# Kernel tuning notes

Hardware: AMD Instinct MI355X
Metric: run time of the kernel (lower is better)

The kernel has to match this reference:

```python
import jax, jax.numpy as jnp
import numpy as np

B, T, C = 4, 2048, 1024
H = 16
HS = C // H

def setup_inputs() -> dict:
    key = jax.random.key(0)
    ks = jax.random.split(key, 5)
    s = 0.02
    return {
        "x": jax.random.normal(ks[0], (B, T, C), dtype=jnp.float32),
        "c_attn_w": jax.random.normal(ks[1], (C, 3 * C), dtype=jnp.float32) * s,
        "c_attn_b": jax.random.normal(ks[2], (3 * C,), dtype=jnp.float32) * s,
        "c_proj_w": jax.random.normal(ks[3], (C, C), dtype=jnp.float32) * s,
        "c_proj_b": jax.random.normal(ks[4], (C,), dtype=jnp.float32) * s,
    }

def reference(x, c_attn_w, c_attn_b, c_proj_w, c_proj_b):
    b, t, c = x.shape
    qkv = x @ c_attn_w + c_attn_b                       # (B,T,3C)
    q, k, v = jnp.split(qkv, 3, axis=2)
    # (B,T,C) -> (B,H,T,hs)
    q = q.reshape(b, t, H, HS).transpose(0, 2, 1, 3)
    k = k.reshape(b, t, H, HS).transpose(0, 2, 1, 3)
    v = v.reshape(b, t, H, HS).transpose(0, 2, 1, 3)
    scale = 1.0 / np.sqrt(HS).astype(np.float32)
    attn = jnp.einsum("bhqd,bhkd->bhqk", q, k) * scale  # (B,H,T,T)
    causal = jnp.tril(jnp.ones((t, t), dtype=bool))
    attn = jnp.where(causal[None, None, :, :], attn, -jnp.inf)
    attn = jax.nn.softmax(attn, axis=-1)
    y = jnp.einsum("bhqk,bhkd->bhqd", attn, v)          # (B,H,T,hs)
    y = y.transpose(0, 2, 1, 3).reshape(b, t, c)        # (B,T,C)
    return y @ c_proj_w + c_proj_b
```

## Files before the change

kernel.cpp:

```cpp
#include <hip/hip_runtime.h>

typedef __attribute__((ext_vector_type(8))) _Float16 h8;
typedef __attribute__((ext_vector_type(4))) _Float16 h4;
typedef __attribute__((ext_vector_type(4))) float f4;
typedef __attribute__((ext_vector_type(16))) float f16x;
typedef __attribute__((ext_vector_type(4))) unsigned u4;

#define MFMA16(a,b,c) __builtin_amdgcn_mfma_f32_16x16x32_f16(a,b,c,0,0,0)
#define MFMA32(a,b,c) __builtin_amdgcn_mfma_f32_32x32x16_f16(a,b,c,0,0,0)

__device__ inline void gload16(const void* g, void* l) {
    __builtin_amdgcn_global_load_lds(
        (const __attribute__((address_space(1))) void*)g,
        (__attribute__((address_space(3))) void*)l, 16, 0, 0);
}

__device__ inline float swap_half(float x) { return __shfl_xor(x, 32, 64); }

__global__ __launch_bounds__(256) void k_f32_to_f16(const float* __restrict__ in,
                                                    _Float16* __restrict__ out, int n4) {
    int i = blockIdx.x * 256 + threadIdx.x;
    if (i < n4) {
        float4 v = ((const float4*)in)[i];
        h4 h;
        h[0] = (_Float16)v.x; h[1] = (_Float16)v.y;
        h[2] = (_Float16)v.z; h[3] = (_Float16)v.w;
        ((h4*)out)[i] = h;
    }
}

__global__ __launch_bounds__(256) void k_transpose_f16(const float* __restrict__ W,
                                                       _Float16* __restrict__ Wt,
                                                       int K, int N) {
    __shared__ float tile[64 * 68];
    const int k0 = blockIdx.x * 64, n0 = blockIdx.y * 64;
    const int t = threadIdx.x;
    const int tr = t >> 4;
    const int tc = t & 15;
#pragma unroll
    for (int i = 0; i < 4; ++i) {
        int r = tr + i * 16;
        float4 v = *(const float4*)(W + (size_t)(k0 + r) * N + n0 + tc * 4);
        *(float4*)(&tile[r * 68 + tc * 4]) = v;
    }
    __syncthreads();
#pragma unroll
    for (int i = 0; i < 4; ++i) {
        int nl = tr + i * 16;
        h4 hv;
#pragma unroll
        for (int j = 0; j < 4; ++j)
            hv[j] = (_Float16)tile[(tc * 4 + j) * 68 + nl];
        *(h4*)(Wt + (size_t)(n0 + nl) * K + k0 + tc * 4) = hv;
    }
}

template <int MODE>
__global__ __launch_bounds__(256) void k_gemm(const _Float16* __restrict__ A,
                                              const _Float16* __restrict__ Bt,
                                              const float* __restrict__ bias,
                                              _Float16* __restrict__ oQ,
                                              _Float16* __restrict__ oK,
                                              _Float16* __restrict__ oV,
                                              float* __restrict__ oF,
                                              int M, int N, int K) {
    __shared__ _Float16 As[2][128 * 32];
    __shared__ _Float16 Bs[2][128 * 32];
    const int tid = threadIdx.x;
    const int lane = tid & 63, wv = tid >> 6;
    const int wm = wv >> 1, wn = wv & 1;
    const int l15 = lane & 15, l4 = lane >> 4;
    const int bm = blockIdx.x * 128, bn = blockIdx.y * 128;
    f4 acc[4][4] = {};

    const int srow = lane >> 2, scol = (lane & 3) * 8;
    const _Float16* Ag = A + (size_t)(bm + srow) * K + scol;
    const _Float16* Bg = Bt + (size_t)(bn + srow) * K + scol;

#pragma unroll
    for (int j = 0; j < 2; ++j) {
        const int rb_ = (wv * 2 + j) * 16;
        gload16(Ag + (size_t)rb_ * K, &As[0][(wv * 2 + j) * 512]);
        gload16(Bg + (size_t)rb_ * K, &Bs[0][(wv * 2 + j) * 512]);
    }
    asm volatile("s_waitcnt vmcnt(0)" ::: "memory");
    __syncthreads();

    int cur = 0;
    for (int k0 = 0; k0 < K; k0 += 32) {
        if (k0 + 32 < K) {
#pragma unroll
            for (int j = 0; j < 2; ++j) {
                const int rb_ = (wv * 2 + j) * 16;
                gload16(Ag + (size_t)rb_ * K + k0 + 32, &As[cur ^ 1][(wv * 2 + j) * 512]);
                gload16(Bg + (size_t)rb_ * K + k0 + 32, &Bs[cur ^ 1][(wv * 2 + j) * 512]);
            }
        }

        const _Float16* Ac = As[cur];
        const _Float16* Bc = Bs[cur];
        h8 af[4], bf[4];
#pragma unroll
        for (int i = 0; i < 4; ++i)
            af[i] = *(const h8*)(&Ac[(wm * 64 + i * 16 + l15) * 32 + l4 * 8]);
#pragma unroll
        for (int i = 0; i < 4; ++i)
            bf[i] = *(const h8*)(&Bc[(wn * 64 + i * 16 + l15) * 32 + l4 * 8]);
        __builtin_amdgcn_s_setprio(1);
#pragma unroll
        for (int mi = 0; mi < 4; ++mi)
#pragma unroll
            for (int ni = 0; ni < 4; ++ni)
                acc[mi][ni] = MFMA16(af[mi], bf[ni], acc[mi][ni]);
        __builtin_amdgcn_s_setprio(0);

        asm volatile("s_waitcnt vmcnt(0)" ::: "memory");
        __syncthreads();
        cur ^= 1;
    }

#pragma unroll
    for (int mi = 0; mi < 4; ++mi) {
#pragma unroll
        for (int ni = 0; ni < 4; ++ni) {
            int col = bn + wn * 64 + ni * 16 + l15;
            float bv = bias[col];
            int rb = bm + wm * 64 + mi * 16 + l4 * 4;
            if (MODE == 0) {
                int which = col >> 10, n1 = col & 1023;
                int hh = n1 >> 6, dd = n1 & 63;
                if (which == 2) {
                    int b = rb >> 11, tq = rb & 2047;
                    h4 pv;
#pragma unroll
                    for (int i = 0; i < 4; ++i) pv[i] = (_Float16)(acc[mi][ni][i] + bv);
                    *(h4*)(oV + ((size_t)(b * 16 + hh) * 64 + dd) * 2048 + tq) = pv;
                } else {
                    _Float16* dst = which == 0 ? oQ : oK;
                    const float scl = which == 0 ? 0.18033688011112042f : 1.0f;
#pragma unroll
                    for (int i = 0; i < 4; ++i) {
                        int row = rb + i;
                        int b = row >> 11, tq = row & 2047;
                        dst[(((size_t)b * 16 + hh) * 2048 + tq) * 64 + dd] =
                            (_Float16)((acc[mi][ni][i] + bv) * scl);
                    }
                }
            } else {
#pragma unroll
                for (int i = 0; i < 4; ++i)
                    oF[(size_t)(rb + i) * N + col] = acc[mi][ni][i] + bv;
            }
        }
    }
}

#define SWZI(row, cb) ((((row) << 7) + ((cb) ^ ((((row) & 7) << 4)))) >> 1)

__global__ __launch_bounds__(64) void k_attn(const _Float16* __restrict__ Qh,
                                             const _Float16* __restrict__ Kh,
                                             const _Float16* __restrict__ Vt,
                                             _Float16* __restrict__ Yh) {
    __shared__ _Float16 lds[8192];
    const int bid = blockIdx.x;
    const int bh = bid & 63;
    const int qb = 63 - (bid >> 6);
    const int t = threadIdx.x;
    const int l31 = t & 31, hi = t >> 5;
    const int h16 = hi * 16, h4o = hi * 4;
    const size_t base = (size_t)bh * 2048 * 64;

    const int qabs = qb * 32 + l31;
    h8 qf[4];
#pragma unroll
    for (int dk = 0; dk < 4; ++dk)
        qf[dk] = *(const h8*)(Qh + base + (size_t)qabs * 64 + dk * 16 + hi * 8);

    f16x O0 = {}, O1 = {};
    float m = -1e30f, l = 0.f;

    const int sr = t >> 3;
    const int sc = (t & 7) * 8;
    const _Float16* Kg = Kh + base + (size_t)sr * 64 + sc;
    const _Float16* Vg = Vt + base + (size_t)sr * 2048 + sc;
    const int kbw = qb >> 1;

    {
        h8 kn[8], vn[8];
#pragma unroll
        for (int j = 0; j < 8; ++j) kn[j] = *(const h8*)(Kg + j * 512);
#pragma unroll
        for (int j = 0; j < 8; ++j) vn[j] = *(const h8*)(Vg + j * 16384);
#pragma unroll
        for (int j = 0; j < 8; ++j) *(h8*)(&lds[SWZI(j * 8 + sr, (t & 7) * 16)]) = kn[j];
#pragma unroll
        for (int j = 0; j < 8; ++j) *(h8*)(&lds[4096 + SWZI(j * 8 + sr, (t & 7) * 16)]) = vn[j];
    }
    asm volatile("s_waitcnt lgkmcnt(0)" ::: "memory");
    __builtin_amdgcn_sched_barrier(0);

    for (int kb = 0; kb <= kbw; ++kb) {
        const bool pre = (kb < kbw);
        h8 kn[8], vn[8];
        if (pre) {
#pragma unroll
            for (int j = 0; j < 8; ++j)
                kn[j] = *(const h8*)(Kg + (size_t)(kb + 1) * 4096 + j * 512);
        }

        f16x S0 = {}, S1 = {};
        __builtin_amdgcn_s_setprio(1);
#pragma unroll
        for (int dk = 0; dk < 4; ++dk) {
            h8 kf0 = *(const h8*)(&lds[SWZI(l31, dk * 32 + h16)]);
            h8 kf1 = *(const h8*)(&lds[SWZI(32 + l31, dk * 32 + h16)]);
            S0 = MFMA32(kf0, qf[dk], S0);
            S1 = MFMA32(kf1, qf[dk], S1);
        }
        __builtin_amdgcn_s_setprio(0);

        if (pre) {
#pragma unroll
            for (int j = 0; j < 8; ++j)
                vn[j] = *(const h8*)(Vg + (size_t)(kb + 1) * 64 + j * 16384);
        }

        if (kb == kbw) {
#pragma unroll
            for (int r = 0; r < 16; ++r) {
                int key = kb * 64 + (r & 3) + 8 * (r >> 2) + h4o;
                if (key > qabs) S0[r] = -1e30f;
                if (key + 32 > qabs) S1[r] = -1e30f;
            }
        }

        float tr[16];
#pragma unroll
        for (int r = 0; r < 16; ++r) tr[r] = fmaxf(S0[r], S1[r]);
#pragma unroll
        for (int st = 8; st >= 1; st >>= 1)
#pragma unroll
            for (int r = 0; r < st; ++r) tr[r] = fmaxf(tr[r], tr[r + st]);
        float pm = fmaxf(tr[0], swap_half(tr[0]));
        if (!__all(pm - m <= 8.f)) {
            float mnew = fmaxf(m, pm);
            float scl = __builtin_amdgcn_exp2f(m - mnew);
            m = mnew;
            l *= scl;
#pragma unroll
            for (int r = 0; r < 16; ++r) { O0[r] *= scl; O1[r] *= scl; }
        }
#pragma unroll
        for (int r = 0; r < 16; ++r) {
            S0[r] = __builtin_amdgcn_exp2f(S0[r] - m);
            S1[r] = __builtin_amdgcn_exp2f(S1[r] - m);
        }
#pragma unroll
        for (int r = 0; r < 16; ++r) tr[r] = S0[r] + S1[r];
#pragma unroll
        for (int st = 8; st >= 1; st >>= 1)
#pragma unroll
            for (int r = 0; r < st; ++r) tr[r] += tr[r + st];
        l += tr[0] + swap_half(tr[0]);

        h8 pb[4];
#pragma unroll
        for (int kk = 0; kk < 4; ++kk) {
            const int bb = (kk & 1) * 8;
            unsigned W0, W1, W2, W3;
            if (kk < 2) {
                W0 = __builtin_bit_cast(unsigned, __builtin_amdgcn_cvt_pkrtz(S0[bb + 0], S0[bb + 1]));
                W1 = __builtin_bit_cast(unsigned, __builtin_amdgcn_cvt_pkrtz(S0[bb + 2], S0[bb + 3]));
                W2 = __builtin_bit_cast(unsigned, __builtin_amdgcn_cvt_pkrtz(S0[bb + 4], S0[bb + 5]));
                W3 = __builtin_bit_cast(unsigned, __builtin_amdgcn_cvt_pkrtz(S0[bb + 6], S0[bb + 7]));
            } else {
                W0 = __builtin_bit_cast(unsigned, __builtin_amdgcn_cvt_pkrtz(S1[bb + 0], S1[bb + 1]));
                W1 = __builtin_bit_cast(unsigned, __builtin_amdgcn_cvt_pkrtz(S1[bb + 2], S1[bb + 3]));
                W2 = __builtin_bit_cast(unsigned, __builtin_amdgcn_cvt_pkrtz(S1[bb + 4], S1[bb + 5]));
                W3 = __builtin_bit_cast(unsigned, __builtin_amdgcn_cvt_pkrtz(S1[bb + 6], S1[bb + 7]));
            }
            unsigned E0 = (unsigned)__shfl_xor((int)(hi ? W0 : W2), 32, 64);
            unsigned E1 = (unsigned)__shfl_xor((int)(hi ? W1 : W3), 32, 64);
            u4 wvv;
            wvv[0] = hi ? E0 : W0;
            wvv[1] = hi ? E1 : W1;
            wvv[2] = hi ? W2 : E0;
            wvv[3] = hi ? W3 : E1;
            pb[kk] = __builtin_bit_cast(h8, wvv);
        }

        __builtin_amdgcn_s_setprio(1);
#pragma unroll
        for (int kk = 0; kk < 4; ++kk) {
            h8 vf0 = *(const h8*)(&lds[4096 + SWZI(l31, kk * 32 + h16)]);
            h8 vf1 = *(const h8*)(&lds[4096 + SWZI(32 + l31, kk * 32 + h16)]);
            O0 = MFMA32(vf0, pb[kk], O0);
            O1 = MFMA32(vf1, pb[kk], O1);
        }
        __builtin_amdgcn_s_setprio(0);

        if (pre) {
            asm volatile("s_waitcnt lgkmcnt(0)" ::: "memory");
            __builtin_amdgcn_sched_barrier(0);
#pragma unroll
            for (int j = 0; j < 8; ++j) *(h8*)(&lds[SWZI(j * 8 + sr, (t & 7) * 16)]) = kn[j];
#pragma unroll
            for (int j = 0; j < 8; ++j) *(h8*)(&lds[4096 + SWZI(j * 8 + sr, (t & 7) * 16)]) = vn[j];
        }
    }

    asm volatile("s_waitcnt lgkmcnt(0)" ::: "memory");
    __builtin_amdgcn_sched_barrier(0);
    {
        float inv = 1.0f / l;
        _Float16* ow = (_Float16*)lds + (size_t)l31 * 72;
#pragma unroll
        for (int rr = 0; rr < 4; ++rr) {
            h4 a, b;
#pragma unroll
            for (int q = 0; q < 4; ++q) {
                a[q] = (_Float16)(O0[rr * 4 + q] * inv);
                b[q] = (_Float16)(O1[rr * 4 + q] * inv);
            }
            *(h4*)(&ow[rr * 8 + h4o]) = a;
            *(h4*)(&ow[32 + rr * 8 + h4o]) = b;
        }
    }
    asm volatile("s_waitcnt lgkmcnt(0)" ::: "memory");
    __builtin_amdgcn_sched_barrier(0);
    {
        const int b = bh >> 4, head = bh & 15;
        const int row = t >> 1;
#pragma unroll
        for (int i = 0; i < 4; ++i) {
            int seg = (t & 1) * 4 + i;
            h8 v = *(const h8*)(&lds[row * 72 + seg * 8]);
            *(h8*)(Yh + ((size_t)(b * 2048 + qb * 32 + row)) * 1024 + head * 64 + seg * 8) = v;
        }
    }
}

extern "C" void kernel_launch(void* const* d_in, const int* in_sizes, int n_in,
                              void* d_out, int out_size, void* d_ws, size_t ws_size,
                              hipStream_t stream) {
    const float* x  = (const float*)d_in[0];
    const float* Wa = (const float*)d_in[1];
    const float* ba = (const float*)d_in[2];
    const float* Wp = (const float*)d_in[3];
    const float* bp = (const float*)d_in[4];
    float* out = (float*)d_out;

    _Float16* ws = (_Float16*)d_ws;
    const size_t SZ_X = (size_t)8192 * 1024;
    const size_t SZ_WA = (size_t)3072 * 1024;
    const size_t SZ_WP = (size_t)1024 * 1024;
    const size_t SZ_H = (size_t)64 * 2048 * 64;
    _Float16* xh  = ws;
    _Float16* WaT = xh + SZ_X;
    _Float16* WpT = WaT + SZ_WA;
    _Float16* Qh  = WpT + SZ_WP;
    _Float16* Kh  = Qh + SZ_H;
    _Float16* Vth = Kh + SZ_H;
    _Float16* Yh  = Vth + SZ_H;

    k_f32_to_f16<<<8192, 256, 0, stream>>>(x, xh, (int)(SZ_X / 4));
    k_transpose_f16<<<dim3(16, 48), 256, 0, stream>>>(Wa, WaT, 1024, 3072);
    k_transpose_f16<<<dim3(16, 16), 256, 0, stream>>>(Wp, WpT, 1024, 1024);
    k_gemm<0><<<dim3(64, 24), 256, 0, stream>>>(xh, WaT, ba, Qh, Kh, Vth, nullptr,
                                                8192, 3072, 1024);
    k_attn<<<4096, 64, 0, stream>>>(Qh, Kh, Vth, Yh);
    k_gemm<1><<<dim3(64, 8), 256, 0, stream>>>(Yh, WpT, bp, nullptr, nullptr, nullptr,
                                               out, 8192, 1024, 1024);
}
```

Baseline: 188.1 us.

## Share K/V tiles across four waves per attention block with 128-query tiles

The attention kernel moves from one 64-thread wave handling 32 queries to a 256-thread block of four waves covering 128 queries. The waves cooperatively load each 64-key K/V tile into LDS and share it, which cuts redundant global K/V traffic by up to fourfold. In exchange it adds __syncthreads barriers per key tile, and waves whose causal range ends earlier sit idle through the final tiles. The output staging is also switched to a swizzled LDS layout for 128 rows.

```diff
diff --git a/kernel.cpp b/kernel.cpp
--- a/kernel.cpp
+++ b/kernel.cpp
@@ -157,20 +157,20 @@
 
 #define SWZI(row, cb) ((((row) << 7) + ((cb) ^ ((((row) & 7) << 4)))) >> 1)
 
-__global__ __launch_bounds__(64) void k_attn(const _Float16* __restrict__ Qh,
-                                             const _Float16* __restrict__ Kh,
-                                             const _Float16* __restrict__ Vt,
-                                             _Float16* __restrict__ Yh) {
+__global__ __launch_bounds__(256) void k_attn(const _Float16* __restrict__ Qh,
+                                              const _Float16* __restrict__ Kh,
+                                              const _Float16* __restrict__ Vt,
+                                              _Float16* __restrict__ Yh) {
     __shared__ _Float16 lds[8192];
     const int bid = blockIdx.x;
     const int bh = bid & 63;
-    const int qb = 63 - (bid >> 6);
-    const int t = threadIdx.x;
-    const int l31 = t & 31, hi = t >> 5;
+    const int qt = 15 - (bid >> 6);
+    const int tid = threadIdx.x, w = tid >> 6;
+    const int l31 = tid & 31, hi = (tid >> 5) & 1;
     const int h16 = hi * 16, h4o = hi * 4;
     const size_t base = (size_t)bh * 2048 * 64;
 
-    const int qabs = qb * 32 + l31;
+    const int qabs = qt * 128 + w * 32 + l31;
     h8 qf[4];
 #pragma unroll
     for (int dk = 0; dk < 4; ++dk)
@@ -179,141 +179,140 @@
     f16x O0 = {}, O1 = {};
     float m = -1e30f, l = 0.f;
 
-    const int sr = t >> 3;
-    const int sc = (t & 7) * 8;
-    const _Float16* Kg = Kh + base + (size_t)sr * 64 + sc;
-    const _Float16* Vg = Vt + base + (size_t)sr * 2048 + sc;
-    const int kbw = qb >> 1;
+    const int sr = tid >> 3;
+    const int sc8 = (tid & 7) * 8;
+    const int scb = (tid & 7) * 16;
+    const int kbb = 2 * qt + 1;
+    const int kbw = 2 * qt + (w >> 1);
 
     {
-        h8 kn[8], vn[8];
-#pragma unroll
-        for (int j = 0; j < 8; ++j) kn[j] = *(const h8*)(Kg + j * 512);
-#pragma unroll
-        for (int j = 0; j < 8; ++j) vn[j] = *(const h8*)(Vg + j * 16384);
-#pragma unroll
-        for (int j = 0; j < 8; ++j) *(h8*)(&lds[SWZI(j * 8 + sr, (t & 7) * 16)]) = kn[j];
-#pragma unroll
-        for (int j = 0; j < 8; ++j) *(h8*)(&lds[4096 + SWZI(j * 8 + sr, (t & 7) * 16)]) = vn[j];
-    }
-    asm volatile("s_waitcnt lgkmcnt(0)" ::: "memory");
-    __builtin_amdgcn_sched_barrier(0);
-
-    for (int kb = 0; kb <= kbw; ++kb) {
-        const bool pre = (kb < kbw);
-        h8 kn[8], vn[8];
+#pragma unroll
+        for (int j = 0; j < 2; ++j) {
+            int row = j * 32 + sr;
+            h8 kv = *(const h8*)(Kh + base + (size_t)row * 64 + sc8);
+            h8 vv = *(const h8*)(Vt + base + (size_t)row * 2048 + sc8);
+            *(h8*)(&lds[SWZI(row, scb)]) = kv;
+            *(h8*)(&lds[4096 + SWZI(row, scb)]) = vv;
+        }
+    }
+    __syncthreads();
+
+    for (int kb = 0; kb <= kbb; ++kb) {
+        const bool pre = (kb < kbb);
+        h8 kn[2], vn[2];
         if (pre) {
 #pragma unroll
-            for (int j = 0; j < 8; ++j)
-                kn[j] = *(const h8*)(Kg + (size_t)(kb + 1) * 4096 + j * 512);
-        }
-
-        f16x S0 = {}, S1 = {};
-        __builtin_amdgcn_s_setprio(1);
-#pragma unroll
-        for (int dk = 0; dk < 4; ++dk) {
-            h8 kf0 = *(const h8*)(&lds[SWZI(l31, dk * 32 + h16)]);
-            h8 kf1 = *(const h8*)(&lds[SWZI(32 + l31, dk * 32 + h16)]);
-            S0 = MFMA32(kf0, qf[dk], S0);
-            S1 = MFMA32(kf1, qf[dk], S1);
-        }
-        __builtin_amdgcn_s_setprio(0);
-
+            for (int j = 0; j < 2; ++j) {
+                int row = j * 32 + sr;
+                kn[j] = *(const h8*)(Kh + base + (size_t)((kb + 1) * 64 + row) * 64 + sc8);
+                vn[j] = *(const h8*)(Vt + base + (size_t)row * 2048 + (kb + 1) * 64 + sc8);
+            }
+        }
+
+        if (kb <= kbw) {
+            f16x S0 = {}, S1 = {};
+            __builtin_amdgcn_s_setprio(1);
+#pragma unroll
+            for (int dk = 0; dk < 4; ++dk) {
+                h8 kf0 = *(const h8*)(&lds[SWZI(l31, dk * 32 + h16)]);
+                h8 kf1 = *(const h8*)(&lds[SWZI(32 + l31, dk * 32 + h16)]);
+                S0 = MFMA32(kf0, qf[dk], S0);
+                S1 = MFMA32(kf1, qf[dk], S1);
+            }
+            __builtin_amdgcn_s_setprio(0);
+
+            if (kb == kbw) {
+#pragma unroll
+                for (int r = 0; r < 16; ++r) {
+                    int key = kb * 64 + (r & 3) + 8 * (r >> 2) + h4o;
+                    if (key > qabs) S0[r] = -1e30f;
+                    if (key + 32 > qabs) S1[r] = -1e30f;
+                }
+            }
+
+            float tr[16];
+#pragma unroll
+            for (int r = 0; r < 16; ++r) tr[r] = fmaxf(S0[r], S1[r]);
+#pragma unroll
+            for (int st = 8; st >= 1; st >>= 1)
+#pragma unroll
+                for (int r = 0; r < st; ++r) tr[r] = fmaxf(tr[r], tr[r + st]);
+            float pm = fmaxf(tr[0], swap_half(tr[0]));
+            if (!__all(pm - m <= 8.f)) {
+                float mnew = fmaxf(m, pm);
+                float scl = __builtin_amdgcn_exp2f(m - mnew);
+                m = mnew;
+                l *= scl;
+#pragma unroll
+                for (int r = 0; r < 16; ++r) { O0[r] *= scl; O1[r] *= scl; }
+            }
+#pragma unroll
+            for (int r = 0; r < 16; ++r) {
+                S0[r] = __builtin_amdgcn_exp2f(S0[r] - m);
+                S1[r] = __builtin_amdgcn_exp2f(S1[r] - m);
+            }
+#pragma unroll
+            for (int r = 0; r < 16; ++r) tr[r] = S0[r] + S1[r];
+#pragma unroll
+            for (int st = 8; st >= 1; st >>= 1)
+#pragma unroll
+                for (int r = 0; r < st; ++r) tr[r] += tr[r + st];
+            l += tr[0] + swap_half(tr[0]);
+
+            h8 pb[4];
+#pragma unroll
+            for (int kk = 0; kk < 4; ++kk) {
+                const int bb = (kk & 1) * 8;
+                unsigned W0, W1, W2, W3;
+                if (kk < 2) {
+                    W0 = __builtin_bit_cast(unsigned, __builtin_amdgcn_cvt_pkrtz(S0[bb + 0], S0[bb + 1]));
+                    W1 = __builtin_bit_cast(unsigned, __builtin_amdgcn_cvt_pkrtz(S0[bb + 2], S0[bb + 3]));
+                    W2 = __builtin_bit_cast(unsigned, __builtin_amdgcn_cvt_pkrtz(S0[bb + 4], S0[bb + 5]));
+                    W3 = __builtin_bit_cast(unsigned, __builtin_amdgcn_cvt_pkrtz(S0[bb + 6], S0[bb + 7]));
+                } else {
+                    W0 = __builtin_bit_cast(unsigned, __builtin_amdgcn_cvt_pkrtz(S1[bb + 0], S1[bb + 1]));
+                    W1 = __builtin_bit_cast(unsigned, __builtin_amdgcn_cvt_pkrtz(S1[bb + 2], S1[bb + 3]));
+                    W2 = __builtin_bit_cast(unsigned, __builtin_amdgcn_cvt_pkrtz(S1[bb + 4], S1[bb + 5]));
+                    W3 = __builtin_bit_cast(unsigned, __builtin_amdgcn_cvt_pkrtz(S1[bb + 6], S1[bb + 7]));
+                }
+                unsigned E0 = (unsigned)__shfl_xor((int)(hi ? W0 : W2), 32, 64);
+                unsigned E1 = (unsigned)__shfl_xor((int)(hi ? W1 : W3), 32, 64);
+                u4 wvv;
+                wvv[0] = hi ? E0 : W0;
+                wvv[1] = hi ? E1 : W1;
+                wvv[2] = hi ? W2 : E0;
+                wvv[3] = hi ? W3 : E1;
+                pb[kk] = __builtin_bit_cast(h8, wvv);
+            }
+
+            __builtin_amdgcn_s_setprio(1);
+#pragma unroll
+            for (int kk = 0; kk < 4; ++kk) {
+                h8 vf0 = *(const h8*)(&lds[4096 + SWZI(l31, kk * 32 + h16)]);
+                h8 vf1 = *(const h8*)(&lds[4096 + SWZI(32 + l31, kk * 32 + h16)]);
+                O0 = MFMA32(vf0, pb[kk], O0);
+                O1 = MFMA32(vf1, pb[kk], O1);
+            }
+            __builtin_amdgcn_s_setprio(0);
+        }
+
+        __syncthreads();
         if (pre) {
 #pragma unroll
-            for (int j = 0; j < 8; ++j)
-                vn[j] = *(const h8*)(Vg + (size_t)(kb + 1) * 64 + j * 16384);
-        }
-
-        if (kb == kbw) {
-#pragma unroll
-            for (int r = 0; r < 16; ++r) {
-                int key = kb * 64 + (r & 3) + 8 * (r >> 2) + h4o;
-                if (key > qabs) S0[r] = -1e30f;
-                if (key + 32 > qabs) S1[r] = -1e30f;
-            }
-        }
-
-        float tr[16];
-#pragma unroll
-        for (int r = 0; r < 16; ++r) tr[r] = fmaxf(S0[r], S1[r]);
-#pragma unroll
-        for (int st = 8; st >= 1; st >>= 1)
-#pragma unroll
-            for (int r = 0; r < st; ++r) tr[r] = fmaxf(tr[r], tr[r + st]);
-        float pm = fmaxf(tr[0], swap_half(tr[0]));
-        if (!__all(pm - m <= 8.f)) {
-            float mnew = fmaxf(m, pm);
-            float scl = __builtin_amdgcn_exp2f(m - mnew);
-            m = mnew;
-            l *= scl;
-#pragma unroll
-            for (int r = 0; r < 16; ++r) { O0[r] *= scl; O1[r] *= scl; }
-        }
-#pragma unroll
-        for (int r = 0; r < 16; ++r) {
-            S0[r] = __builtin_amdgcn_exp2f(S0[r] - m);
-            S1[r] = __builtin_amdgcn_exp2f(S1[r] - m);
-        }
-#pragma unroll
-        for (int r = 0; r < 16; ++r) tr[r] = S0[r] + S1[r];
-#pragma unroll
-        for (int st = 8; st >= 1; st >>= 1)
-#pragma unroll
-            for (int r = 0; r < st; ++r) tr[r] += tr[r + st];
-        l += tr[0] + swap_half(tr[0]);
-
-        h8 pb[4];
-#pragma unroll
-        for (int kk = 0; kk < 4; ++kk) {
-            const int bb = (kk & 1) * 8;
-            unsigned W0, W1, W2, W3;
-            if (kk < 2) {
-                W0 = __builtin_bit_cast(unsigned, __builtin_amdgcn_cvt_pkrtz(S0[bb + 0], S0[bb + 1]));
-                W1 = __builtin_bit_cast(unsigned, __builtin_amdgcn_cvt_pkrtz(S0[bb + 2], S0[bb + 3]));
-                W2 = __builtin_bit_cast(unsigned, __builtin_amdgcn_cvt_pkrtz(S0[bb + 4], S0[bb + 5]));
-                W3 = __builtin_bit_cast(unsigned, __builtin_amdgcn_cvt_pkrtz(S0[bb + 6], S0[bb + 7]));
-            } else {
-                W0 = __builtin_bit_cast(unsigned, __builtin_amdgcn_cvt_pkrtz(S1[bb + 0], S1[bb + 1]));
-                W1 = __builtin_bit_cast(unsigned, __builtin_amdgcn_cvt_pkrtz(S1[bb + 2], S1[bb + 3]));
-                W2 = __builtin_bit_cast(unsigned, __builtin_amdgcn_cvt_pkrtz(S1[bb + 4], S1[bb + 5]));
-                W3 = __builtin_bit_cast(unsigned, __builtin_amdgcn_cvt_pkrtz(S1[bb + 6], S1[bb + 7]));
-            }
-            unsigned E0 = (unsigned)__shfl_xor((int)(hi ? W0 : W2), 32, 64);
-            unsigned E1 = (unsigned)__shfl_xor((int)(hi ? W1 : W3), 32, 64);
-            u4 wvv;
-            wvv[0] = hi ? E0 : W0;
-            wvv[1] = hi ? E1 : W1;
-            wvv[2] = hi ? W2 : E0;
-            wvv[3] = hi ? W3 : E1;
-            pb[kk] = __builtin_bit_cast(h8, wvv);
-        }
-
-        __builtin_amdgcn_s_setprio(1);
-#pragma unroll
-        for (int kk = 0; kk < 4; ++kk) {
-            h8 vf0 = *(const h8*)(&lds[4096 + SWZI(l31, kk * 32 + h16)]);
-            h8 vf1 = *(const h8*)(&lds[4096 + SWZI(32 + l31, kk * 32 + h16)]);
-            O0 = MFMA32(vf0, pb[kk], O0);
-            O1 = MFMA32(vf1, pb[kk], O1);
-        }
-        __builtin_amdgcn_s_setprio(0);
-
-        if (pre) {
-            asm volatile("s_waitcnt lgkmcnt(0)" ::: "memory");
-            __builtin_amdgcn_sched_barrier(0);
-#pragma unroll
-            for (int j = 0; j < 8; ++j) *(h8*)(&lds[SWZI(j * 8 + sr, (t & 7) * 16)]) = kn[j];
-#pragma unroll
-            for (int j = 0; j < 8; ++j) *(h8*)(&lds[4096 + SWZI(j * 8 + sr, (t & 7) * 16)]) = vn[j];
-        }
-    }
-
-    asm volatile("s_waitcnt lgkmcnt(0)" ::: "memory");
-    __builtin_amdgcn_sched_barrier(0);
+            for (int j = 0; j < 2; ++j) {
+                int row = j * 32 + sr;
+                *(h8*)(&lds[SWZI(row, scb)]) = kn[j];
+                *(h8*)(&lds[4096 + SWZI(row, scb)]) = vn[j];
+            }
+            __syncthreads();
+        }
+    }
+
+    __syncthreads();
+
     {
         float inv = 1.0f / l;
-        _Float16* ow = (_Float16*)lds + (size_t)l31 * 72;
+        const int R = w * 32 + l31;
 #pragma unroll
         for (int rr = 0; rr < 4; ++rr) {
             h4 a, b;
@@ -322,20 +321,19 @@
                 a[q] = (_Float16)(O0[rr * 4 + q] * inv);
                 b[q] = (_Float16)(O1[rr * 4 + q] * inv);
             }
-            *(h4*)(&ow[rr * 8 + h4o]) = a;
-            *(h4*)(&ow[32 + rr * 8 + h4o]) = b;
-        }
-    }
-    asm volatile("s_waitcnt lgkmcnt(0)" ::: "memory");
-    __builtin_amdgcn_sched_barrier(0);
+            *(h4*)(&lds[SWZI(R, rr * 16 + hi * 8)]) = a;
+            *(h4*)(&lds[SWZI(R, 64 + rr * 16 + hi * 8)]) = b;
+        }
+    }
+    __syncthreads();
     {
         const int b = bh >> 4, head = bh & 15;
-        const int row = t >> 1;
+        const int row = tid >> 1;
 #pragma unroll
         for (int i = 0; i < 4; ++i) {
-            int seg = (t & 1) * 4 + i;
-            h8 v = *(const h8*)(&lds[row * 72 + seg * 8]);
-            *(h8*)(Yh + ((size_t)(b * 2048 + qb * 32 + row)) * 1024 + head * 64 + seg * 8) = v;
+            int seg = (tid & 1) * 4 + i;
+            h8 v = *(const h8*)(&lds[SWZI(row, seg * 16)]);
+            *(h8*)(Yh + ((size_t)(b * 2048 + qt * 128 + row)) * 1024 + head * 64 + seg * 8) = v;
         }
     }
 }
@@ -368,7 +366,7 @@
     k_transpose_f16<<<dim3(16, 16), 256, 0, stream>>>(Wp, WpT, 1024, 1024);
     k_gemm<0><<<dim3(64, 24), 256, 0, stream>>>(xh, WaT, ba, Qh, Kh, Vth, nullptr,
                                                 8192, 3072, 1024);
-    k_attn<<<4096, 64, 0, stream>>>(Qh, Kh, Vth, Yh);
+    k_attn<<<1024, 256, 0, stream>>>(Qh, Kh, Vth, Yh);
     k_gemm<1><<<dim3(64, 8), 256, 0, stream>>>(Yh, WpT, bp, nullptr, nullptr, nullptr,
                                                out, 8192, 1024, 1024);
 }
```

New measurement: 181.5 us (median of 2 runs). 1.04x faster.
